# Performance work log

Measured on AMD Instinct MI355X. Metric: run time of the kernel, lower is better.

## Reference

```python
import jax, jax.numpy as jnp
import numpy as np

B, W, S, D, H = 16, 128, 16, 768, 12
HD = D // H

def _ln(x, g, b):
    m = x.mean(-1, keepdims=True)
    v = ((x - m) ** 2).mean(-1, keepdims=True)
    return (x - m) / jnp.sqrt(v + 1e-5) * g + b

def _lin(x, w, b):
    return x @ w.T + b

def _rope(t):
    # t: (N, H, L, HD); interleaved even/odd rotation, base 10000
    inv = 1.0 / (10000.0 ** (jnp.arange(0, HD, 2, dtype=jnp.float32) / HD))
    fr = jnp.arange(t.shape[2], dtype=jnp.float32)[:, None] * inv[None, :]  # (L, HD//2)
    cos, sin = jnp.cos(fr), jnp.sin(fr)
    te, to = t[..., ::2], t[..., 1::2]
    return jnp.stack([te * cos - to * sin, te * sin + to * cos], -1).reshape(t.shape)

def _mha(q, k, v, mask=None):
    # q,k,v: (N, H, L, HD)
    s = jnp.einsum('nhqd,nhkd->nhqk', q, k) / jnp.sqrt(jnp.float32(HD))
    if mask is not None:
        s = jnp.where(mask[None, None], -jnp.inf, s)
    a = jax.nn.softmax(s, axis=-1)
    return jnp.einsum('nhqk,nhkd->nhqd', a, v)

def _heads(t, L):
    return t.reshape(-1, L, H, HD).transpose(0, 2, 1, 3)

def setup_inputs() -> dict:
    key = jax.random.key(0)
    ks = jax.random.split(key, 16)
    def w(i, shape):
        return jax.random.normal(ks[i], shape, jnp.float32) * 0.02
    return {
        'x': jax.random.normal(ks[0], (B, W, S, D), jnp.float32),
        'causal_mask': jnp.triu(jnp.ones((W, W), dtype=bool), k=1),
        'sn_g': jnp.ones((D,), jnp.float32), 'sn_b': jnp.zeros((D,), jnp.float32),
        'sa_in_w': w(1, (3 * D, D)), 'sa_in_b': jnp.zeros((3 * D,), jnp.float32),
        'sa_out_w': w(2, (D, D)), 'sa_out_b': jnp.zeros((D,), jnp.float32),
        'tn_g': jnp.ones((D,), jnp.float32), 'tn_b': jnp.zeros((D,), jnp.float32),
        'tq_w': w(3, (D, D)), 'tq_b': jnp.zeros((D,), jnp.float32),
        'tk_w': w(4, (D, D)), 'tk_b': jnp.zeros((D,), jnp.float32),
        'tv_w': w(5, (D, D)), 'tv_b': jnp.zeros((D,), jnp.float32),
        'to_w': w(6, (D, D)), 'to_b': jnp.zeros((D,), jnp.float32),
        'fn_g': jnp.ones((D,), jnp.float32), 'fn_b': jnp.zeros((D,), jnp.float32),
        'f1_w': w(7, (4 * D, D)), 'f1_b': jnp.zeros((4 * D,), jnp.float32),
        'f2_w': w(8, (D, 4 * D)), 'f2_b': jnp.zeros((D,), jnp.float32),
    }

def reference(x, causal_mask, sn_g, sn_b, sa_in_w, sa_in_b, sa_out_w, sa_out_b,
              tn_g, tn_b, tq_w, tq_b, tk_w, tk_b, tv_w, tv_b, to_w, to_b,
              fn_g, fn_b, f1_w, f1_b, f2_w, f2_b):
    # ---- spatial attention within each timestep: (B*W, S, D) ----
    xs = x.reshape(B * W, S, D)
    xn = _ln(xs, sn_g, sn_b)
    q, k, v = jnp.split(_lin(xn, sa_in_w, sa_in_b), 3, axis=-1)
    o = _mha(_heads(q, S), _heads(k, S), _heads(v, S))
    o = o.transpose(0, 2, 1, 3).reshape(B * W, S, D)
    xs = xs + _lin(o, sa_out_w, sa_out_b)
    x = xs.reshape(B, W, S, D)
    # ---- causal temporal attention with RoPE: (B*S, W, D) ----
    xt = x.transpose(0, 2, 1, 3).reshape(B * S, W, D)
    xn = _ln(xt, tn_g, tn_b)
    q = _rope(_heads(_lin(xn, tq_w, tq_b), W))
    k = _rope(_heads(_lin(xn, tk_w, tk_b), W))
    v = _heads(_lin(xn, tv_w, tv_b), W)
    o = _mha(q, k, v, causal_mask)
    o = o.transpose(0, 2, 1, 3).reshape(B * S, W, D)
    xt = xt + _lin(o, to_w, to_b)
    x = xt.reshape(B, S, W, D).transpose(0, 2, 1, 3)
    # ---- feed-forward (exact GELU, as torch default) ----
    h = jax.nn.gelu(_lin(_ln(x, fn_g, fn_b), f1_w, f1_b), approximate=False)
    return x + _lin(h, f2_w, f2_b)
```

## Files before the change

kernel.cpp:

```cpp
#include <hip/hip_runtime.h>
#include <stdint.h>


#define NB 16
#define NW 128
#define NS 16
#define ND 768
#define NH 12
#define NTOK 32768

typedef __attribute__((ext_vector_type(8))) short short8;
typedef __attribute__((ext_vector_type(4))) float f32x4;

__device__ __forceinline__ float blo(unsigned v){ return __builtin_bit_cast(float, v << 16); }
__device__ __forceinline__ float bhi(unsigned v){ return __builtin_bit_cast(float, v & 0xffff0000u); }
__device__ __forceinline__ float bus(unsigned short u){ return __builtin_bit_cast(float, ((unsigned)u) << 16); }
__device__ __forceinline__ unsigned short f2b(float f){
  unsigned u = __builtin_bit_cast(unsigned, f);
  u += 0x7fffu + ((u >> 16) & 1u);
  return (unsigned short)(u >> 16);
}
__device__ __forceinline__ void gld_lds16(const void* g, void* l){
  __builtin_amdgcn_global_load_lds((const __attribute__((address_space(1))) void*)g,
                                   (__attribute__((address_space(3))) void*)l, 16, 0, 0);
}

__global__ __launch_bounds__(256) void convert_k(const float* __restrict__ in,
                                                 unsigned short* __restrict__ out, int n4){
  int i = blockIdx.x * 256 + threadIdx.x;
  int stride = gridDim.x * 256;
  for (; i < n4; i += stride){
    float4 v = ((const float4*)in)[i];
    unsigned lo = (unsigned)f2b(v.x) | ((unsigned)f2b(v.y) << 16);
    unsigned hi = (unsigned)f2b(v.z) | ((unsigned)f2b(v.w) << 16);
    ((uint2*)out)[i] = make_uint2(lo, hi);
  }
}

__global__ __launch_bounds__(256) void concat3_k(const float* __restrict__ a, const float* __restrict__ b,
                                                 const float* __restrict__ c, float* __restrict__ o){
  int i = blockIdx.x * 256 + threadIdx.x;
  if (i < 768){ o[i] = a[i]; o[768 + i] = b[i]; o[1536 + i] = c[i]; }
}

__global__ __launch_bounds__(256) void rope_k(float* __restrict__ tab){
  int i = blockIdx.x * 256 + threadIdx.x;
  if (i < 128 * 32){
    int w = i >> 5, p = i & 31;
    float inv = powf(10000.0f, -((float)(2 * p)) / 64.0f);
    float ang = (float)w * inv;
    tab[i * 2] = cosf(ang);
    tab[i * 2 + 1] = sinf(ang);
  }
}

template<int INF32>
__global__ __launch_bounds__(256) void ln_k(const void* __restrict__ xin, const float* __restrict__ g,
                                            const float* __restrict__ bt, unsigned short* __restrict__ out){
  const int row = blockIdx.x;
  const int t = threadIdx.x;
  const float* xf = (const float*)xin;
  const unsigned short* xb = (const unsigned short*)xin;
  float v[3];
#pragma unroll
  for (int i = 0; i < 3; ++i){
    int j = t + i * 256;
    v[i] = INF32 ? xf[(size_t)row * 768 + j] : bus(xb[(size_t)row * 768 + j]);
  }
  float s = v[0] + v[1] + v[2];
  float ss = v[0]*v[0] + v[1]*v[1] + v[2]*v[2];
#pragma unroll
  for (int o = 1; o < 64; o <<= 1){ s += __shfl_xor(s, o, 64); ss += __shfl_xor(ss, o, 64); }
  __shared__ float red[8];
  int w = t >> 6;
  if ((t & 63) == 0){ red[w*2] = s; red[w*2+1] = ss; }
  __syncthreads();
  s = red[0] + red[2] + red[4] + red[6];
  ss = red[1] + red[3] + red[5] + red[7];
  float mean = s * (1.0f / 768.0f);
  float var = ss * (1.0f / 768.0f) - mean * mean;
  float rstd = rsqrtf(var + 1e-5f);
#pragma unroll
  for (int i = 0; i < 3; ++i){
    int j = t + i * 256;
    out[(size_t)row * 768 + j] = f2b((v[i] - mean) * rstd * g[j] + bt[j]);
  }
}

template<int MODE>
__global__ __launch_bounds__(256, 3) void gemm128_k(const unsigned short* __restrict__ A,
                                                    const unsigned short* __restrict__ Bw,
                                                    const float* __restrict__ bias,
                                                    const void* __restrict__ resid,
                                                    void* __restrict__ outp, int K, int M){
  __shared__ char LB[49152];
  char* const Asl = LB;
  char* const Bsl = LB + 24576;
  const int tid = threadIdx.x;
  const int lane = tid & 63, w = tid >> 6;
  const int llo = lane & 15, lhi = lane >> 4;
  const int wm = w >> 1, wn = w & 1;
  const int NT = K >> 5;

  const int gx = gridDim.x;
  const int nwg = gx * gridDim.y;
  const int orig = blockIdx.y * gx + blockIdx.x;
  const int lin = (nwg & 7) ? orig : ((orig & 7) * (nwg >> 3) + (orig >> 3));
  const int by = lin / gx, bx = lin - by * gx;
  const int brow = by << 7;
  const int bcol = bx << 7;

  const int r0 = tid >> 2, cp = tid & 3;
  const int swz = (cp << 4) ^ ((r0 & 3) << 4);
  const char* aG = (const char*)(A + (size_t)(brow + r0) * K) + swz;
  const char* bG = (const char*)(Bw + (size_t)(bcol + r0) * K) + swz;
  const int J2 = K * 128;
  const int ldst = w << 10;

  auto stage = [&](const char* g, int gb, char* slotbase){
    gld_lds16(g + gb,      slotbase + ldst);
    gld_lds16(g + gb + J2, slotbase + ldst + (1 << 12));
  };

  short8 a[4], b[4];
  auto rd_a = [&](const char* Ab){
#pragma unroll
    for (int mi = 0; mi < 4; ++mi){
      const int rr = (wm << 6) + (mi << 4) + llo;
      a[mi] = *(const short8*)(Ab + rr * 64 + ((lhi << 4) ^ ((rr & 3) << 4)));
    }
  };
  auto rd_b2 = [&](const char* Bb, int nb){
#pragma unroll
    for (int ni = 0; ni < 2; ++ni){
      const int cc = (wn << 6) + ((nb + ni) << 4) + llo;
      b[nb + ni] = *(const short8*)(Bb + cc * 64 + ((lhi << 4) ^ ((cc & 3) << 4)));
    }
  };

  f32x4 acc[4][4];
#pragma unroll
  for (int m = 0; m < 4; ++m)
#pragma unroll
    for (int n = 0; n < 4; ++n) acc[m][n] = f32x4{0.f, 0.f, 0.f, 0.f};

  auto mfma_h = [&](int nb){
    __builtin_amdgcn_s_setprio(1);
#pragma unroll
    for (int mi = 0; mi < 4; ++mi)
#pragma unroll
      for (int ni = 0; ni < 2; ++ni)
        acc[mi][nb + ni] = __builtin_amdgcn_mfma_f32_16x16x32_bf16(b[nb + ni], a[mi], acc[mi][nb + ni], 0, 0, 0);
    __builtin_amdgcn_s_setprio(0);
  };

  stage(aG, 0,  Asl);
  stage(bG, 0,  Bsl);
  stage(aG, 64, Asl + 8192);
  stage(bG, 64, Bsl + 8192);
  asm volatile("s_waitcnt vmcnt(4)" ::: "memory");
  __builtin_amdgcn_s_barrier();

  int sl = 0;
  for (int t = 0; t < NT; ++t){
    const char* Ab = Asl + (sl << 13);
    const char* Bb = Bsl + (sl << 13);
    int sl2 = sl + 2; if (sl2 >= 3) sl2 -= 3;
    const int tb = t << 6;

    rd_b2(Bb, 0);
    rd_a(Ab);
    if (t + 2 < NT) stage(aG, tb + 128, Asl + (sl2 << 13));
    __builtin_amdgcn_s_barrier();
    asm volatile("s_waitcnt lgkmcnt(0)" ::: "memory");
    mfma_h(0);
    __builtin_amdgcn_s_barrier();

    rd_b2(Bb, 2);
    if (t + 2 < NT) stage(bG, tb + 128, Bsl + (sl2 << 13));
    __builtin_amdgcn_s_barrier();
    asm volatile("s_waitcnt lgkmcnt(0)" ::: "memory");
    mfma_h(2);
    if (t + 2 < NT) asm volatile("s_waitcnt vmcnt(4)" ::: "memory");
    else            asm volatile("s_waitcnt vmcnt(0)" ::: "memory");
    __builtin_amdgcn_s_barrier();

    sl = sl + 1; if (sl >= 3) sl = 0;
  }

  const int orow = brow + (wm << 6);
  const int ocol = bcol + (wn << 6);
  const unsigned short* resb = (const unsigned short*)resid;
  const float* resf = (const float*)resid;
#pragma unroll
  for (int m = 0; m < 4; ++m){
    const int row = orow + (m << 4) + llo;
    const size_t rb = (size_t)row * M;
#pragma unroll
    for (int n = 0; n < 4; ++n){
      const int col = ocol + (n << 4) + (lhi << 2);
      const float4 bv = *(const float4*)&bias[col];
      float v0 = acc[m][n][0] + bv.x;
      float v1 = acc[m][n][1] + bv.y;
      float v2 = acc[m][n][2] + bv.z;
      float v3 = acc[m][n][3] + bv.w;
      const size_t off = rb + col;
      if (MODE == 1){
        float y0 = v0 * (1.5957691216f + 0.0713548163f * v0 * v0);
        float y1 = v1 * (1.5957691216f + 0.0713548163f * v1 * v1);
        float y2 = v2 * (1.5957691216f + 0.0713548163f * v2 * v2);
        float y3 = v3 * (1.5957691216f + 0.0713548163f * v3 * v3);
        v0 = v0 / (1.0f + __expf(-y0));
        v1 = v1 / (1.0f + __expf(-y1));
        v2 = v2 / (1.0f + __expf(-y2));
        v3 = v3 / (1.0f + __expf(-y3));
      } else if (MODE == 2){
        const float4 rv = *(const float4*)&resf[off];
        v0 += rv.x; v1 += rv.y; v2 += rv.z; v3 += rv.w;
      } else if (MODE == 3 || MODE == 4){
        const uint2 rv = *(const uint2*)&resb[off];
        v0 += blo(rv.x); v1 += bhi(rv.x); v2 += blo(rv.y); v3 += bhi(rv.y);
      }
      if (MODE == 4){
        float4 ov; ov.x = v0; ov.y = v1; ov.z = v2; ov.w = v3;
        *(float4*)&((float*)outp)[off] = ov;
      } else {
        unsigned lo = (unsigned)f2b(v0) | ((unsigned)f2b(v1) << 16);
        unsigned hi = (unsigned)f2b(v2) | ((unsigned)f2b(v3) << 16);
        *(uint2*)&((unsigned short*)outp)[off] = make_uint2(lo, hi);
      }
    }
  }
}

__global__ __launch_bounds__(256) void sattn_k(const unsigned short* __restrict__ qkv,
                                               unsigned short* __restrict__ o){
  const int bw = blockIdx.x, h = blockIdx.y;
  const int t = threadIdx.x;
  __shared__ unsigned short qh[16 * 68], kh[16 * 68], vh[16 * 68];
  __shared__ float pl[16 * 17];
  const int row = t >> 4, c4 = t & 15;
  const size_t base = ((size_t)(bw * 16 + row)) * 2304 + h * 64 + c4 * 4;
  *(uint2*)&qh[row * 68 + c4 * 4] = *(const uint2*)&qkv[base];
  *(uint2*)&kh[row * 68 + c4 * 4] = *(const uint2*)&qkv[base + 768];
  *(uint2*)&vh[row * 68 + c4 * 4] = *(const uint2*)&qkv[base + 1536];
  __syncthreads();

  const int q = row, k = c4;
  float s = 0.f;
#pragma unroll
  for (int c = 0; c < 16; ++c){
    uint2 qv = *(const uint2*)&qh[q * 68 + c * 4];
    uint2 kv = *(const uint2*)&kh[k * 68 + c * 4];
    s += blo(qv.x) * blo(kv.x) + bhi(qv.x) * bhi(kv.x);
    s += blo(qv.y) * blo(kv.y) + bhi(qv.y) * bhi(kv.y);
  }
  s *= 0.125f;
  float m = s;
#pragma unroll
  for (int off = 1; off < 16; off <<= 1) m = fmaxf(m, __shfl_xor(m, off, 64));
  float p = __expf(s - m);
  float su = p;
#pragma unroll
  for (int off = 1; off < 16; off <<= 1) su += __shfl_xor(su, off, 64);
  pl[q * 17 + k] = p / su;
  __syncthreads();

  float o0 = 0.f, o1 = 0.f, o2 = 0.f, o3 = 0.f;
#pragma unroll
  for (int kk = 0; kk < 16; ++kk){
    float pw = pl[q * 17 + kk];
    uint2 vv = *(const uint2*)&vh[kk * 68 + c4 * 4];
    o0 += pw * blo(vv.x); o1 += pw * bhi(vv.x);
    o2 += pw * blo(vv.y); o3 += pw * bhi(vv.y);
  }
  const size_t ob = ((size_t)(bw * 16 + q)) * 768 + h * 64 + c4 * 4;
  unsigned r0 = (unsigned)f2b(o0) | ((unsigned)f2b(o1) << 16);
  unsigned r1 = (unsigned)f2b(o2) | ((unsigned)f2b(o3) << 16);
  *(uint2*)&o[ob] = make_uint2(r0, r1);
}

__global__ __launch_bounds__(256) void tattn_k(const unsigned short* __restrict__ qkv,
                                               const float* __restrict__ rope,
                                               unsigned short* __restrict__ o){
  const int bs = blockIdx.x, h = blockIdx.y;
  const int b = bs >> 4, s = bs & 15;
  const int t = threadIdx.x, lane = t & 63, w = t >> 6;
  const int lhi = lane >> 4, llo = lane & 15;
  __shared__ unsigned short Qs[128 * 64];
  __shared__ unsigned short Ks[128 * 64];
  __shared__ unsigned short Vt[64 * 128];
  __shared__ unsigned short P[128 * 128];

  {
    const int r = t >> 1;
    const int dbase = (t & 1) * 32;
    const size_t tokb = ((size_t)((b * 128 + r) * 16 + s)) * 2304 + h * 64;
    const float2* rp = (const float2*)rope;
#pragma unroll
    for (int mch = 0; mch < 4; ++mch){
      const int d0 = dbase + mch * 8;
      uint4 qv = *(const uint4*)&qkv[tokb + d0];
      uint4 kv = *(const uint4*)&qkv[tokb + 768 + d0];
      uint4 vv = *(const uint4*)&qkv[tokb + 1536 + d0];
      unsigned qin[4] = {qv.x, qv.y, qv.z, qv.w};
      unsigned kin[4] = {kv.x, kv.y, kv.z, kv.w};
      unsigned qo[4], ko[4];
#pragma unroll
      for (int j = 0; j < 4; ++j){
        float2 cssn = rp[r * 32 + (d0 >> 1) + j];
        float cs = cssn.x, sn = cssn.y;
        float qe = blo(qin[j]), qd = bhi(qin[j]);
        float ke = blo(kin[j]), kd = bhi(kin[j]);
        qo[j] = (unsigned)f2b(qe * cs - qd * sn) | ((unsigned)f2b(qe * sn + qd * cs) << 16);
        ko[j] = (unsigned)f2b(ke * cs - kd * sn) | ((unsigned)f2b(ke * sn + kd * cs) << 16);
      }
      const int byq = r * 128 + ((d0 * 2) ^ ((r & 7) << 4));
      *(uint4*)((char*)Qs + byq) = make_uint4(qo[0], qo[1], qo[2], qo[3]);
      *(uint4*)((char*)Ks + byq) = make_uint4(ko[0], ko[1], ko[2], ko[3]);
      unsigned vin[4] = {vv.x, vv.y, vv.z, vv.w};
#pragma unroll
      for (int j = 0; j < 8; ++j){
        const int d = d0 + j;
        unsigned short val = (j & 1) ? (unsigned short)(vin[j >> 1] >> 16)
                                     : (unsigned short)(vin[j >> 1] & 0xffffu);
        *(unsigned short*)((char*)Vt + d * 256 + ((r * 2) ^ ((d & 7) << 4))) = val;
      }
    }
  }
  __syncthreads();

  const int qbase = w * 32;
  f32x4 st[8][2];
#pragma unroll
  for (int i = 0; i < 8; ++i){ st[i][0] = f32x4{0.f,0.f,0.f,0.f}; st[i][1] = f32x4{0.f,0.f,0.f,0.f}; }
#pragma unroll
  for (int kd = 0; kd < 2; ++kd){
    short8 bq[2];
#pragma unroll
    for (int fq = 0; fq < 2; ++fq){
      const int qr = qbase + fq * 16 + llo;
      bq[fq] = *(const short8*)((const char*)Qs + qr * 128 + ((kd * 64 + lhi * 16) ^ ((qr & 7) << 4)));
    }
#pragma unroll
    for (int fk = 0; fk < 8; ++fk){
      const int kr = fk * 16 + llo;
      short8 ak = *(const short8*)((const char*)Ks + kr * 128 + ((kd * 64 + lhi * 16) ^ ((kr & 7) << 4)));
      st[fk][0] = __builtin_amdgcn_mfma_f32_16x16x32_bf16(ak, bq[0], st[fk][0], 0, 0, 0);
      st[fk][1] = __builtin_amdgcn_mfma_f32_16x16x32_bf16(ak, bq[1], st[fk][1], 0, 0, 0);
    }
  }

#pragma unroll
  for (int fq = 0; fq < 2; ++fq){
    const int qg = qbase + fq * 16 + llo;
    float m = -1e30f;
#pragma unroll
    for (int fk = 0; fk < 8; ++fk)
#pragma unroll
      for (int rr = 0; rr < 4; ++rr){
        const int kg = fk * 16 + lhi * 4 + rr;
        float sv = (kg <= qg) ? st[fk][fq][rr] : -1e30f;
        st[fk][fq][rr] = sv;
        m = fmaxf(m, sv);
      }
    m = fmaxf(m, __shfl_xor(m, 16, 64));
    m = fmaxf(m, __shfl_xor(m, 32, 64));
    float su = 0.f;
#pragma unroll
    for (int fk = 0; fk < 8; ++fk)
#pragma unroll
      for (int rr = 0; rr < 4; ++rr){
        float p = __expf((st[fk][fq][rr] - m) * 0.125f);
        st[fk][fq][rr] = p;
        su += p;
      }
    su += __shfl_xor(su, 16, 64);
    su += __shfl_xor(su, 32, 64);
    const float rs = 1.0f / su;
#pragma unroll
    for (int fk = 0; fk < 8; ++fk){
      const int kk = fk * 16 + lhi * 4;
      unsigned lo = (unsigned)f2b(st[fk][fq][0] * rs) | ((unsigned)f2b(st[fk][fq][1] * rs) << 16);
      unsigned hi = (unsigned)f2b(st[fk][fq][2] * rs) | ((unsigned)f2b(st[fk][fq][3] * rs) << 16);
      *(uint2*)((char*)P + qg * 256 + ((kk * 2) ^ ((qg & 7) << 4))) = make_uint2(lo, hi);
    }
  }
  __syncthreads();

  f32x4 oacc[2][4];
#pragma unroll
  for (int i = 0; i < 2; ++i)
#pragma unroll
    for (int j = 0; j < 4; ++j) oacc[i][j] = f32x4{0.f,0.f,0.f,0.f};
#pragma unroll
  for (int ks = 0; ks < 4; ++ks){
    short8 pa[2];
#pragma unroll
    for (int fq = 0; fq < 2; ++fq){
      const int qr = qbase + fq * 16 + llo;
      pa[fq] = *(const short8*)((const char*)P + qr * 256 + ((ks * 64 + lhi * 16) ^ ((qr & 7) << 4)));
    }
#pragma unroll
    for (int fd = 0; fd < 4; ++fd){
      const int dr = fd * 16 + llo;
      short8 vb = *(const short8*)((const char*)Vt + dr * 256 + ((ks * 64 + lhi * 16) ^ ((dr & 7) << 4)));
      oacc[0][fd] = __builtin_amdgcn_mfma_f32_16x16x32_bf16(pa[0], vb, oacc[0][fd], 0, 0, 0);
      oacc[1][fd] = __builtin_amdgcn_mfma_f32_16x16x32_bf16(pa[1], vb, oacc[1][fd], 0, 0, 0);
    }
  }

#pragma unroll
  for (int fq = 0; fq < 2; ++fq)
#pragma unroll
    for (int fd = 0; fd < 4; ++fd)
#pragma unroll
      for (int rr = 0; rr < 4; ++rr){
        const int qg = qbase + fq * 16 + lhi * 4 + rr;
        const int d = fd * 16 + llo;
        const size_t ob = ((size_t)((b * 128 + qg) * 16 + s)) * 768 + h * 64 + d;
        o[ob] = f2b(oacc[fq][fd][rr]);
      }
}

__global__ __launch_bounds__(256) void sentinel_k(float* out){
  if (blockIdx.x == 0 && threadIdx.x == 0) out[0] = 12345.0f;
}

extern "C" void kernel_launch(void* const* d_in, const int* in_sizes, int n_in,
                              void* d_out, int out_size, void* d_ws, size_t ws_size,
                              hipStream_t stream){
  const float* x       = (const float*)d_in[0];
  const float* sn_g    = (const float*)d_in[2];
  const float* sn_b    = (const float*)d_in[3];
  const float* sa_in_w = (const float*)d_in[4];
  const float* sa_in_b = (const float*)d_in[5];
  const float* sa_out_w= (const float*)d_in[6];
  const float* sa_out_b= (const float*)d_in[7];
  const float* tn_g    = (const float*)d_in[8];
  const float* tn_b    = (const float*)d_in[9];
  const float* tq_w    = (const float*)d_in[10];
  const float* tq_b    = (const float*)d_in[11];
  const float* tk_w    = (const float*)d_in[12];
  const float* tk_b    = (const float*)d_in[13];
  const float* tv_w    = (const float*)d_in[14];
  const float* tv_b    = (const float*)d_in[15];
  const float* to_w    = (const float*)d_in[16];
  const float* to_b    = (const float*)d_in[17];
  const float* fn_g    = (const float*)d_in[18];
  const float* fn_b    = (const float*)d_in[19];
  const float* f1_w    = (const float*)d_in[20];
  const float* f1_b    = (const float*)d_in[21];
  const float* f2_w    = (const float*)d_in[22];
  const float* f2_b    = (const float*)d_in[23];

  char* ws = (char*)d_ws;
  size_t off = 0;
  auto alloc = [&](size_t bytes) -> void* {
    void* p = ws + off;
    off += (bytes + 255) & ~(size_t)255;
    return p;
  };
  unsigned short* Wqkv = (unsigned short*)alloc((size_t)2304*768*2);
  unsigned short* Wo1  = (unsigned short*)alloc((size_t)768*768*2);
  unsigned short* W3   = (unsigned short*)alloc((size_t)2304*768*2);
  float*          b3   = (float*)alloc(2304*4);
  unsigned short* Wto  = (unsigned short*)alloc((size_t)768*768*2);
  unsigned short* Wf1  = (unsigned short*)alloc((size_t)3072*768*2);
  unsigned short* Wf2  = (unsigned short*)alloc((size_t)768*3072*2);
  float*          rope = (float*)alloc(128*32*2*4);
  unsigned short* xn   = (unsigned short*)alloc((size_t)NTOK*768*2);
  unsigned short* qkv  = (unsigned short*)alloc((size_t)NTOK*3072*2);
  unsigned short* xs2  = (unsigned short*)alloc((size_t)NTOK*768*2);
  unsigned short* xt2  = (unsigned short*)alloc((size_t)NTOK*768*2);
  unsigned short* ob   = xn;

  if (ws_size < off){ sentinel_k<<<1, 64, 0, stream>>>((float*)d_out); return; }

  convert_k<<<1024, 256, 0, stream>>>(sa_in_w, Wqkv, 2304*768/4);
  convert_k<<<512, 256, 0, stream>>>(sa_out_w, Wo1, 768*768/4);
  convert_k<<<512, 256, 0, stream>>>(tq_w, W3, 768*768/4);
  convert_k<<<512, 256, 0, stream>>>(tk_w, W3 + 768*768, 768*768/4);
  convert_k<<<512, 256, 0, stream>>>(tv_w, W3 + 2*768*768, 768*768/4);
  concat3_k<<<3, 256, 0, stream>>>(tq_b, tk_b, tv_b, b3);
  convert_k<<<512, 256, 0, stream>>>(to_w, Wto, 768*768/4);
  convert_k<<<1024, 256, 0, stream>>>(f1_w, Wf1, 3072*768/4);
  convert_k<<<1024, 256, 0, stream>>>(f2_w, Wf2, 768*3072/4);
  rope_k<<<16, 256, 0, stream>>>(rope);

  ln_k<1><<<NTOK, 256, 0, stream>>>(x, sn_g, sn_b, xn);
  gemm128_k<0><<<dim3(18, 256), 256, 0, stream>>>(xn, Wqkv, sa_in_b, nullptr, qkv, 768, 2304);
  sattn_k<<<dim3(2048, 12), 256, 0, stream>>>(qkv, ob);
  gemm128_k<2><<<dim3(6, 256), 256, 0, stream>>>(ob, Wo1, sa_out_b, x, xs2, 768, 768);

  ln_k<0><<<NTOK, 256, 0, stream>>>(xs2, tn_g, tn_b, xn);
  gemm128_k<0><<<dim3(18, 256), 256, 0, stream>>>(xn, W3, b3, nullptr, qkv, 768, 2304);
  tattn_k<<<dim3(256, 12), 256, 0, stream>>>(qkv, rope, ob);
  gemm128_k<3><<<dim3(6, 256), 256, 0, stream>>>(ob, Wto, to_b, xs2, xt2, 768, 768);

  ln_k<0><<<NTOK, 256, 0, stream>>>(xt2, fn_g, fn_b, xn);
  gemm128_k<1><<<dim3(24, 256), 256, 0, stream>>>(xn, Wf1, f1_b, nullptr, qkv, 768, 3072);
  gemm128_k<4><<<dim3(6, 256), 256, 0, stream>>>(qkv, Wf2, f2_b, xt2, d_out, 3072, 768);
}
```

Before: 1.147 ms.

## Replace triple-buffered GEMM pipeline with single-buffer loop and fuse weight conversions

Rewrites the GEMM main loop to drop the three-slot prefetch pipeline. Each K-step now loads one 32-wide tile into a 16KB LDS buffer with a new XOR swizzle, syncs, and runs all 16 MFMAs, allowing 4 blocks per CU instead of 3. It also changes the block-to-XCD remapping to group row tiles. The eight weight-conversion launches are merged into one kernel. The result trades explicit load/compute overlap for higher occupancy, so global-load latency is now exposed inside each block.

```diff
diff --git a/kernel.cpp b/kernel.cpp
--- a/kernel.cpp
+++ b/kernel.cpp
@@ -25,15 +25,31 @@
                                    (__attribute__((address_space(3))) void*)l, 16, 0, 0);
 }
 
-__global__ __launch_bounds__(256) void convert_k(const float* __restrict__ in,
-                                                 unsigned short* __restrict__ out, int n4){
+__global__ __launch_bounds__(256) void convertall_k(
+    const float* __restrict__ s0, const float* __restrict__ s1, const float* __restrict__ s2,
+    const float* __restrict__ s3, const float* __restrict__ s4, const float* __restrict__ s5,
+    const float* __restrict__ s6, const float* __restrict__ s7,
+    unsigned short* __restrict__ d0, unsigned short* __restrict__ d1, unsigned short* __restrict__ d2,
+    unsigned short* __restrict__ d3, unsigned short* __restrict__ d4, unsigned short* __restrict__ d5,
+    unsigned short* __restrict__ d6, unsigned short* __restrict__ d7){
+  const int n0 = 442368, n1 = 147456, n2 = 147456, n3 = 147456, n4 = 147456, n5 = 147456, n6 = 589824, n7 = 589824;
+  const int c0 = n0, c1 = c0+n1, c2 = c1+n2, c3 = c2+n3, c4 = c3+n4, c5 = c4+n5, c6 = c5+n6, c7 = c6+n7;
   int i = blockIdx.x * 256 + threadIdx.x;
-  int stride = gridDim.x * 256;
-  for (; i < n4; i += stride){
-    float4 v = ((const float4*)in)[i];
+  const int stride = gridDim.x * 256;
+  for (; i < c7; i += stride){
+    const float* s; unsigned short* d; int j;
+    if      (i < c0){ s = s0; d = d0; j = i; }
+    else if (i < c1){ s = s1; d = d1; j = i - c0; }
+    else if (i < c2){ s = s2; d = d2; j = i - c1; }
+    else if (i < c3){ s = s3; d = d3; j = i - c2; }
+    else if (i < c4){ s = s4; d = d4; j = i - c3; }
+    else if (i < c5){ s = s5; d = d5; j = i - c4; }
+    else if (i < c6){ s = s6; d = d6; j = i - c5; }
+    else            { s = s7; d = d7; j = i - c6; }
+    float4 v = ((const float4*)s)[j];
     unsigned lo = (unsigned)f2b(v.x) | ((unsigned)f2b(v.y) << 16);
     unsigned hi = (unsigned)f2b(v.z) | ((unsigned)f2b(v.w) << 16);
-    ((uint2*)out)[i] = make_uint2(lo, hi);
+    ((uint2*)d)[j] = make_uint2(lo, hi);
   }
 }
 
@@ -88,55 +104,60 @@
 }
 
 template<int MODE>
-__global__ __launch_bounds__(256, 3) void gemm128_k(const unsigned short* __restrict__ A,
-                                                    const unsigned short* __restrict__ Bw,
-                                                    const float* __restrict__ bias,
-                                                    const void* __restrict__ resid,
-                                                    void* __restrict__ outp, int K, int M){
-  __shared__ char LB[49152];
-  char* const Asl = LB;
-  char* const Bsl = LB + 24576;
+__global__ __launch_bounds__(256, 4) void gemm97_k(const unsigned short* __restrict__ A,
+                                                   const unsigned short* __restrict__ Bw,
+                                                   const float* __restrict__ bias,
+                                                   const void* __restrict__ resid,
+                                                   void* __restrict__ outp, int K, int M){
+  __shared__ char LB[16384];
+  char* const As = LB;
+  char* const Bs = LB + 8192;
   const int tid = threadIdx.x;
   const int lane = tid & 63, w = tid >> 6;
   const int llo = lane & 15, lhi = lane >> 4;
   const int wm = w >> 1, wn = w & 1;
   const int NT = K >> 5;
 
-  const int gx = gridDim.x;
-  const int nwg = gx * gridDim.y;
+  const int gx = gridDim.x, gy = gridDim.y;
+  const int nwg = gx * gy;
   const int orig = blockIdx.y * gx + blockIdx.x;
-  const int lin = (nwg & 7) ? orig : ((orig & 7) * (nwg >> 3) + (orig >> 3));
-  const int by = lin / gx, bx = lin - by * gx;
-  const int brow = by << 7;
-  const int bcol = bx << 7;
-
-  const int r0 = tid >> 2, cp = tid & 3;
-  const int swz = (cp << 4) ^ ((r0 & 3) << 4);
-  const char* aG = (const char*)(A + (size_t)(brow + r0) * K) + swz;
-  const char* bG = (const char*)(Bw + (size_t)(bcol + r0) * K) + swz;
-  const int J2 = K * 128;
+  int bxx, byy;
+  if (((nwg & 7) == 0) && ((gy & 63) == 0)){
+    const int xcd = orig & 7, idx = orig >> 3;
+    const int grpsz = gx << 3;
+    const int g = idx / grpsz, rem = idx - g * grpsz;
+    bxx = rem >> 3;
+    byy = xcd * (gy >> 3) + (g << 3) + (rem & 7);
+  } else {
+    byy = orig / gx; bxx = orig - byy * gx;
+  }
+  const int brow = byy << 7;
+  const int bcol = bxx << 7;
+
+  const int lineb = tid >> 3, cfb = tid & 7;
+  const int cfs = cfb ^ (lineb & 7);
+  const int srow = 2 * lineb + (cfs >> 2);
+  const int skc = cfs & 3;
+  const char* pa = (const char*)(A + (size_t)(brow + srow) * K + skc * 8);
+  const char* pb = (const char*)(Bw + (size_t)(bcol + srow) * K + skc * 8);
+  const int rowJ = K * 128;
   const int ldst = w << 10;
 
-  auto stage = [&](const char* g, int gb, char* slotbase){
-    gld_lds16(g + gb,      slotbase + ldst);
-    gld_lds16(g + gb + J2, slotbase + ldst + (1 << 12));
-  };
-
-  short8 a[4], b[4];
-  auto rd_a = [&](const char* Ab){
-#pragma unroll
-    for (int mi = 0; mi < 4; ++mi){
-      const int rr = (wm << 6) + (mi << 4) + llo;
-      a[mi] = *(const short8*)(Ab + rr * 64 + ((lhi << 4) ^ ((rr & 3) << 4)));
-    }
-  };
-  auto rd_b2 = [&](const char* Bb, int nb){
-#pragma unroll
-    for (int ni = 0; ni < 2; ++ni){
-      const int cc = (wn << 6) + ((nb + ni) << 4) + llo;
-      b[nb + ni] = *(const short8*)(Bb + cc * 64 + ((lhi << 4) ^ ((cc & 3) << 4)));
-    }
-  };
+  int aoff[4], boff[4];
+#pragma unroll
+  for (int mi = 0; mi < 4; ++mi){
+    const int rr = (wm << 6) + (mi << 4) + llo;
+    const int line = rr >> 1;
+    const int pos = ((((rr & 1) << 2) | lhi)) ^ (line & 7);
+    aoff[mi] = line * 128 + pos * 16;
+  }
+#pragma unroll
+  for (int ni = 0; ni < 4; ++ni){
+    const int cc = (wn << 6) + (ni << 4) + llo;
+    const int line = cc >> 1;
+    const int pos = ((((cc & 1) << 2) | lhi)) ^ (line & 7);
+    boff[ni] = line * 128 + pos * 16;
+  }
 
   f32x4 acc[4][4];
 #pragma unroll
@@ -144,48 +165,27 @@
 #pragma unroll
     for (int n = 0; n < 4; ++n) acc[m][n] = f32x4{0.f, 0.f, 0.f, 0.f};
 
-  auto mfma_h = [&](int nb){
+  for (int t = 0; t < NT; ++t){
+    gld_lds16(pa,        As + ldst);
+    gld_lds16(pa + rowJ, As + ldst + 4096);
+    gld_lds16(pb,        Bs + ldst);
+    gld_lds16(pb + rowJ, Bs + ldst + 4096);
+    pa += 64; pb += 64;
+    __syncthreads();
+    short8 a[4], b[4];
+#pragma unroll
+    for (int i = 0; i < 4; ++i){
+      a[i] = *(const short8*)(As + aoff[i]);
+      b[i] = *(const short8*)(Bs + boff[i]);
+    }
     __builtin_amdgcn_s_setprio(1);
 #pragma unroll
     for (int mi = 0; mi < 4; ++mi)
 #pragma unroll
-      for (int ni = 0; ni < 2; ++ni)
-        acc[mi][nb + ni] = __builtin_amdgcn_mfma_f32_16x16x32_bf16(b[nb + ni], a[mi], acc[mi][nb + ni], 0, 0, 0);
+      for (int ni = 0; ni < 4; ++ni)
+        acc[mi][ni] = __builtin_amdgcn_mfma_f32_16x16x32_bf16(b[ni], a[mi], acc[mi][ni], 0, 0, 0);
     __builtin_amdgcn_s_setprio(0);
-  };
-
-  stage(aG, 0,  Asl);
-  stage(bG, 0,  Bsl);
-  stage(aG, 64, Asl + 8192);
-  stage(bG, 64, Bsl + 8192);
-  asm volatile("s_waitcnt vmcnt(4)" ::: "memory");
-  __builtin_amdgcn_s_barrier();
-
-  int sl = 0;
-  for (int t = 0; t < NT; ++t){
-    const char* Ab = Asl + (sl << 13);
-    const char* Bb = Bsl + (sl << 13);
-    int sl2 = sl + 2; if (sl2 >= 3) sl2 -= 3;
-    const int tb = t << 6;
-
-    rd_b2(Bb, 0);
-    rd_a(Ab);
-    if (t + 2 < NT) stage(aG, tb + 128, Asl + (sl2 << 13));
-    __builtin_amdgcn_s_barrier();
-    asm volatile("s_waitcnt lgkmcnt(0)" ::: "memory");
-    mfma_h(0);
-    __builtin_amdgcn_s_barrier();
-
-    rd_b2(Bb, 2);
-    if (t + 2 < NT) stage(bG, tb + 128, Bsl + (sl2 << 13));
-    __builtin_amdgcn_s_barrier();
-    asm volatile("s_waitcnt lgkmcnt(0)" ::: "memory");
-    mfma_h(2);
-    if (t + 2 < NT) asm volatile("s_waitcnt vmcnt(4)" ::: "memory");
-    else            asm volatile("s_waitcnt vmcnt(0)" ::: "memory");
-    __builtin_amdgcn_s_barrier();
-
-    sl = sl + 1; if (sl >= 3) sl = 0;
+    __syncthreads();
   }
 
   const int orow = brow + (wm << 6);
@@ -477,28 +477,22 @@
 
   if (ws_size < off){ sentinel_k<<<1, 64, 0, stream>>>((float*)d_out); return; }
 
-  convert_k<<<1024, 256, 0, stream>>>(sa_in_w, Wqkv, 2304*768/4);
-  convert_k<<<512, 256, 0, stream>>>(sa_out_w, Wo1, 768*768/4);
-  convert_k<<<512, 256, 0, stream>>>(tq_w, W3, 768*768/4);
-  convert_k<<<512, 256, 0, stream>>>(tk_w, W3 + 768*768, 768*768/4);
-  convert_k<<<512, 256, 0, stream>>>(tv_w, W3 + 2*768*768, 768*768/4);
+  convertall_k<<<2048, 256, 0, stream>>>(sa_in_w, sa_out_w, tq_w, tk_w, tv_w, to_w, f1_w, f2_w,
+                                         Wqkv, Wo1, W3, W3 + 768*768, W3 + 2*768*768, Wto, Wf1, Wf2);
   concat3_k<<<3, 256, 0, stream>>>(tq_b, tk_b, tv_b, b3);
-  convert_k<<<512, 256, 0, stream>>>(to_w, Wto, 768*768/4);
-  convert_k<<<1024, 256, 0, stream>>>(f1_w, Wf1, 3072*768/4);
-  convert_k<<<1024, 256, 0, stream>>>(f2_w, Wf2, 768*3072/4);
   rope_k<<<16, 256, 0, stream>>>(rope);
 
   ln_k<1><<<NTOK, 256, 0, stream>>>(x, sn_g, sn_b, xn);
-  gemm128_k<0><<<dim3(18, 256), 256, 0, stream>>>(xn, Wqkv, sa_in_b, nullptr, qkv, 768, 2304);
+  gemm97_k<0><<<dim3(18, 256), 256, 0, stream>>>(xn, Wqkv, sa_in_b, nullptr, qkv, 768, 2304);
   sattn_k<<<dim3(2048, 12), 256, 0, stream>>>(qkv, ob);
-  gemm128_k<2><<<dim3(6, 256), 256, 0, stream>>>(ob, Wo1, sa_out_b, x, xs2, 768, 768);
+  gemm97_k<2><<<dim3(6, 256), 256, 0, stream>>>(ob, Wo1, sa_out_b, x, xs2, 768, 768);
 
   ln_k<0><<<NTOK, 256, 0, stream>>>(xs2, tn_g, tn_b, xn);
-  gemm128_k<0><<<dim3(18, 256), 256, 0, stream>>>(xn, W3, b3, nullptr, qkv, 768, 2304);
+  gemm97_k<0><<<dim3(18, 256), 256, 0, stream>>>(xn, W3, b3, nullptr, qkv, 768, 2304);
   tattn_k<<<dim3(256, 12), 256, 0, stream>>>(qkv, rope, ob);
-  gemm128_k<3><<<dim3(6, 256), 256, 0, stream>>>(ob, Wto, to_b, xs2, xt2, 768, 768);
+  gemm97_k<3><<<dim3(6, 256), 256, 0, stream>>>(ob, Wto, to_b, xs2, xt2, 768, 768);
 
   ln_k<0><<<NTOK, 256, 0, stream>>>(xt2, fn_g, fn_b, xn);
-  gemm128_k<1><<<dim3(24, 256), 256, 0, stream>>>(xn, Wf1, f1_b, nullptr, qkv, 768, 3072);
-  gemm128_k<4><<<dim3(6, 256), 256, 0, stream>>>(qkv, Wf2, f2_b, xt2, d_out, 3072, 768);
-}
+  gemm97_k<1><<<dim3(24, 256), 256, 0, stream>>>(xn, Wf1, f1_b, nullptr, qkv, 768, 3072);
+  gemm97_k<4><<<dim3(6, 256), 256, 0, stream>>>(qkv, Wf2, f2_b, xt2, d_out, 3072, 768);
+}
```

New measurement: 1.111 ms. 1.03x faster.
